# Optimization experiments

Measured on AMD Instinct MI355X. Metric: run time of the kernel, lower is better.

## Reference

```python
import jax, jax.numpy as jnp
import numpy as np

P, L, E, D, NL, FF = 1024, 32, 512, 768, 6, 3072
H_PA, H_TR = 4, 8
VOCAB = 256


def layer_norm(x, w, b, eps=1e-5):
    mu = x.mean(-1, keepdims=True)
    var = ((x - mu) ** 2).mean(-1, keepdims=True)
    return (x - mu) / jnp.sqrt(var + eps) * w + b


def mha(x, wqkv, bqkv, wo, bo, nheads, key_mask=None):
    # x: [B,S,E]; torch nn.MultiheadAttention semantics (scale q by 1/sqrt(d))
    B, S, Emb = x.shape
    d = Emb // nheads
    qkv = x @ wqkv.T + bqkv
    q, k, v = jnp.split(qkv, 3, axis=-1)
    hd = lambda t: t.reshape(B, S, nheads, d).transpose(0, 2, 1, 3)
    q, k, v = hd(q) * (d ** -0.5), hd(k), hd(v)
    scores = jnp.einsum('bhqd,bhkd->bhqk', q, k)
    if key_mask is not None:
        scores = jnp.where(key_mask[:, None, None, :], scores, -1e9)
    a = jax.nn.softmax(scores, axis=-1)
    o = jnp.einsum('bhqk,bhkd->bhqd', a, v).transpose(0, 2, 1, 3).reshape(B, S, Emb)
    return o @ wo.T + bo


def setup_inputs() -> dict:
    key = jax.random.key(0)
    ks = jax.random.split(key, 32)
    n = lambda i, shape, s=0.02: (jax.random.normal(ks[i], shape, dtype=jnp.float32) * s)
    x = lambda i, shape: jax.random.normal(ks[i], shape, dtype=jnp.float32) * (1.0 / np.sqrt(shape[-1]))
    tokens = jax.random.randint(ks[0], (P, L), 0, VOCAB, dtype=jnp.int32)
    lengths = jax.random.randint(ks[1], (P,), 4, L + 1, dtype=jnp.int32)
    byte_emb = n(2, (VOCAB, E)).at[0].set(0.0)  # padding_idx=0
    inp = {
        'tokens': tokens, 'lengths': lengths,
        'byte_emb': byte_emb,
        'local_pos_emb': n(3, (L, E)),
        'patch_pos_emb': n(4, (P, D)),
        'pa_qkv_w': x(5, (3 * E, E)), 'pa_qkv_b': jnp.zeros((3 * E,), jnp.float32),
        'pa_out_w': x(6, (E, E)), 'pa_out_b': jnp.zeros((E,), jnp.float32),
        'proj_w': x(7, (D, E)), 'proj_b': jnp.zeros((D,), jnp.float32),
        'layers_qkv_w': x(8, (NL, 3 * D, D)), 'layers_qkv_b': jnp.zeros((NL, 3 * D), jnp.float32),
        'layers_out_w': x(9, (NL, D, D)), 'layers_out_b': jnp.zeros((NL, D), jnp.float32),
        'layers_ln1_w': jnp.ones((NL, D), jnp.float32), 'layers_ln1_b': jnp.zeros((NL, D), jnp.float32),
        'layers_ln2_w': jnp.ones((NL, D), jnp.float32), 'layers_ln2_b': jnp.zeros((NL, D), jnp.float32),
        'layers_ff1_w': x(10, (NL, FF, D)), 'layers_ff1_b': jnp.zeros((NL, FF), jnp.float32),
        'layers_ff2_w': x(11, (NL, D, FF)), 'layers_ff2_b': jnp.zeros((NL, D), jnp.float32),
        'ln_f_w': jnp.ones((D,), jnp.float32), 'ln_f_b': jnp.zeros((D,), jnp.float32),
    }
    return inp


def reference(tokens, lengths, byte_emb, local_pos_emb, patch_pos_emb,
              pa_qkv_w, pa_qkv_b, pa_out_w, pa_out_b, proj_w, proj_b,
              layers_qkv_w, layers_qkv_b, layers_out_w, layers_out_b,
              layers_ln1_w, layers_ln1_b, layers_ln2_w, layers_ln2_b,
              layers_ff1_w, layers_ff1_b, layers_ff2_w, layers_ff2_b,
              ln_f_w, ln_f_b):
    mask = jnp.arange(L) < lengths[:, None]  # [P,L] valid-byte mask
    # encode_patches: byte embed + local positions, zero padded slots
    emb = byte_emb[tokens] + local_pos_emb[None, :, :]  # [P,L,E]
    emb = emb * mask[..., None].astype(emb.dtype)
    # per-patch MHA over bytes (key padding mask), vectorized across patches
    attn = mha(emb, pa_qkv_w, pa_qkv_b, pa_out_w, pa_out_b, H_PA, key_mask=mask)
    cnt = mask.sum(-1, keepdims=True).astype(emb.dtype)
    patch_repr = (attn * mask[..., None].astype(emb.dtype)).sum(1) / cnt  # [P,E] masked mean
    # project to hidden and add patch-level positions
    h = patch_repr @ proj_w.T + proj_b + patch_pos_emb[:P]
    h = h[None]  # [1,P,D]
    # pre-norm transformer encoder, gelu FFN
    for i in range(NL):
        hn = layer_norm(h, layers_ln1_w[i], layers_ln1_b[i])
        h = h + mha(hn, layers_qkv_w[i], layers_qkv_b[i], layers_out_w[i], layers_out_b[i], H_TR)
        hn = layer_norm(h, layers_ln2_w[i], layers_ln2_b[i])
        ff = jax.nn.gelu(hn @ layers_ff1_w[i].T + layers_ff1_b[i], approximate=False)
        h = h + ff @ layers_ff2_w[i].T + layers_ff2_b[i]
    return layer_norm(h, ln_f_w, ln_f_b)[0]  # [P,D]
```

## Files before the change

### kernel.cpp

```cpp
#include <hip/hip_runtime.h>
#include <hip/hip_bf16.h>
#include <math.h>

typedef __hip_bfloat16 bf16;
typedef unsigned short u16;
typedef __attribute__((ext_vector_type(8))) short short8;
typedef __attribute__((ext_vector_type(4))) float f32x4;
typedef __attribute__((ext_vector_type(4))) unsigned u32x4;

#define PP 1024
#define LL 32
#define EE 512
#define DD 768
#define NLAYER 6
#define FFDIM 3072

__device__ __forceinline__ float bf2f(u16 u) { return __uint_as_float(((unsigned)u) << 16); }
__device__ __forceinline__ u16 f2b(float x) {
  unsigned u = __float_as_uint(x);
  return (u16)((u + 0x7FFFu + ((u >> 16) & 1u)) >> 16);
}

__global__ __launch_bounds__(256) void cvt4(
    const float* s0, const float* s1, const float* s2, const float* s3,
    u16* d0, u16* d1, u16* d2, u16* d3,
    int n0, int n1, int n2, int n3)
{
  int r = blockIdx.y;
  const float* s = r == 0 ? s0 : r == 1 ? s1 : r == 2 ? s2 : s3;
  u16* d        = r == 0 ? d0 : r == 1 ? d1 : r == 2 ? d2 : d3;
  int n4        = r == 0 ? n0 : r == 1 ? n1 : r == 2 ? n2 : n3;
  int i = blockIdx.x * 256 + threadIdx.x;
  if (i < n4) {
    float4 v = ((const float4*)s)[i];
    ushort4 o;
    o.x = f2b(v.x); o.y = f2b(v.y); o.z = f2b(v.z); o.w = f2b(v.w);
    ((ushort4*)d)[i] = o;
  }
}

__global__ __launch_bounds__(256) void embed_table(
    const float* __restrict__ be, const float* __restrict__ lp, bf16* __restrict__ T)
{
  int i = blockIdx.x * 256 + threadIdx.x;
  int r = i >> 6, c = (i & 63) << 3;
  int t = r >> 5, l = r & 31;
  const float* bp = be + ((long)t << 9) + c;
  const float* pp = lp + ((long)l << 9) + c;
  float4 x0 = *(const float4*)bp, x1 = *(const float4*)(bp + 4);
  float4 y0 = *(const float4*)pp, y1 = *(const float4*)(pp + 4);
  short8 o;
  o[0] = (short)f2b(x0.x + y0.x); o[1] = (short)f2b(x0.y + y0.y);
  o[2] = (short)f2b(x0.z + y0.z); o[3] = (short)f2b(x0.w + y0.w);
  o[4] = (short)f2b(x1.x + y1.x); o[5] = (short)f2b(x1.y + y1.y);
  o[6] = (short)f2b(x1.z + y1.z); o[7] = (short)f2b(x1.w + y1.w);
  *(short8*)((u16*)T + ((long)r << 9) + c) = o;
}

__global__ __launch_bounds__(256) void gemm64(
    const bf16* A, long sAb, int lda,
    const bf16* B, long sBb, int ldb,
    float* Cf, bf16* Cb, long sCb, int ldc,
    const float* bias, int biasStride,
    const float* addf,
    int M, int N, int K, int act)
{
  __shared__ u16 As[2][64][72];
  __shared__ u16 Bs[2][64][72];
  const int bz = blockIdx.z;
  const u16* Ap = (const u16*)A + (long)bz * sAb;
  const u16* Bp = (const u16*)B + (long)bz * sBb;
  const long coff = (long)bz * sCb;
  const int m0 = blockIdx.x << 6, n0 = blockIdx.y << 6;
  const int tid = threadIdx.x;
  const int wave = tid >> 6, lane = tid & 63;
  const int sr = tid >> 3;
  const int scc = (tid & 7) << 3;
  const int br0 = n0 + sr, br1 = n0 + sr + 32;
  const short8 zz = {0,0,0,0,0,0,0,0};
  f32x4 acc[4] = {{0.f,0.f,0.f,0.f},{0.f,0.f,0.f,0.f},{0.f,0.f,0.f,0.f},{0.f,0.f,0.f,0.f}};

  {
    int ch = K < 64 ? K : 64;
    bool kv = scc < ch;
    short8 a0 = zz, a1 = zz, b0 = zz, b1 = zz;
    if (kv) {
      a0 = *(const short8*)(Ap + (long)(m0 + sr) * lda + scc);
      a1 = *(const short8*)(Ap + (long)(m0 + sr + 32) * lda + scc);
      if (br0 < N) b0 = *(const short8*)(Bp + (long)br0 * ldb + scc);
      if (br1 < N) b1 = *(const short8*)(Bp + (long)br1 * ldb + scc);
    }
    *(short8*)&As[0][sr][scc] = a0;
    *(short8*)&As[0][sr + 32][scc] = a1;
    *(short8*)&Bs[0][sr][scc] = b0;
    *(short8*)&Bs[0][sr + 32][scc] = b1;
  }
  __syncthreads();

  const int arow = (wave << 4) + (lane & 15);
  const int kq = (lane >> 4) << 3;
  int buf = 0;
  for (int k0 = 0; k0 < K; k0 += 64) {
    int knext = k0 + 64;
    bool more = knext < K;
    short8 a0 = zz, a1 = zz, b0 = zz, b1 = zz;
    if (more) {
      int ch = K - knext; if (ch > 64) ch = 64;
      bool kv = scc < ch;
      if (kv) {
        a0 = *(const short8*)(Ap + (long)(m0 + sr) * lda + knext + scc);
        a1 = *(const short8*)(Ap + (long)(m0 + sr + 32) * lda + knext + scc);
        if (br0 < N) b0 = *(const short8*)(Bp + (long)br0 * ldb + knext + scc);
        if (br1 < N) b1 = *(const short8*)(Bp + (long)br1 * ldb + knext + scc);
      }
    }
    int rem = K - k0; if (rem > 64) rem = 64;
    {
      short8 af = *(const short8*)&As[buf][arow][kq];
#pragma unroll
      for (int nt = 0; nt < 4; nt++) {
        short8 bfr = *(const short8*)&Bs[buf][(nt << 4) + (lane & 15)][kq];
        acc[nt] = __builtin_amdgcn_mfma_f32_16x16x32_bf16(af, bfr, acc[nt], 0, 0, 0);
      }
    }
    if (rem > 32) {
      short8 af = *(const short8*)&As[buf][arow][32 + kq];
#pragma unroll
      for (int nt = 0; nt < 4; nt++) {
        short8 bfr = *(const short8*)&Bs[buf][(nt << 4) + (lane & 15)][32 + kq];
        acc[nt] = __builtin_amdgcn_mfma_f32_16x16x32_bf16(af, bfr, acc[nt], 0, 0, 0);
      }
    }
    if (more) {
      int nb = buf ^ 1;
      *(short8*)&As[nb][sr][scc] = a0;
      *(short8*)&As[nb][sr + 32][scc] = a1;
      *(short8*)&Bs[nb][sr][scc] = b0;
      *(short8*)&Bs[nb][sr + 32][scc] = b1;
      __syncthreads();
      buf = nb;
    }
  }

  int rbase = m0 + (wave << 4) + ((lane >> 4) << 2);
#pragma unroll
  for (int nt = 0; nt < 4; nt++) {
    int c = n0 + (nt << 4) + (lane & 15);
    if (c >= N) continue;
    float bvl = bias ? bias[bz * biasStride + c] : 0.f;
    if (act == 2 && bz != 0) bvl = 0.f;
#pragma unroll
    for (int j = 0; j < 4; j++) {
      int r = rbase + j;
      long idx = coff + (long)r * ldc + c;
      float v = acc[nt][j] + bvl;
      if (addf) v += addf[idx];
      if (act == 1) v = 0.5f * v * (1.f + erff(v * 0.70710678118654752f));
      if (Cf) Cf[idx] = v;
      if (Cb) Cb[idx] = __float2bfloat16(v);
    }
  }
}

__global__ __launch_bounds__(128) void fused_attn(
    const bf16* __restrict__ qkvt,
    const bf16* __restrict__ Vt,
    bf16* __restrict__ attn)
{
  const int h = blockIdx.y;
  const int wid = threadIdx.x >> 6;
  const int lane = threadIdx.x & 63;
  const int q0 = (blockIdx.x << 5) + (wid << 4);
  const int lr = lane & 15;
  const int lq = lane >> 4;
  const float scale = 0.10206207261596577f;

  const u16* qp = (const u16*)qkvt;
  const u16* kp = qp + 768 + h * 96 + (lq << 3);
  const u16* vp = (const u16*)Vt + ((long)(h * 96 + lr) << 10) + (lq << 3);

  short8 qf[3];
#pragma unroll
  for (int c = 0; c < 3; c++)
    qf[c] = *(const short8*)(qp + (long)(q0 + lr) * 2304 + h * 96 + (c << 5) + (lq << 3));

  f32x4 o[6] = {{0.f,0.f,0.f,0.f},{0.f,0.f,0.f,0.f},{0.f,0.f,0.f,0.f},
                {0.f,0.f,0.f,0.f},{0.f,0.f,0.f,0.f},{0.f,0.f,0.f,0.f}};
  float m = -INFINITY, l = 0.f;

  for (int k0 = 0; k0 < 1024; k0 += 32) {
    f32x4 s0 = {0.f,0.f,0.f,0.f}, s1 = {0.f,0.f,0.f,0.f};
#pragma unroll
    for (int c = 0; c < 3; c++) {
      short8 kf0 = *(const short8*)(kp + (long)(k0 + lr) * 2304 + (c << 5));
      short8 kf1 = *(const short8*)(kp + (long)(k0 + 16 + lr) * 2304 + (c << 5));
      s0 = __builtin_amdgcn_mfma_f32_16x16x32_bf16(kf0, qf[c], s0, 0, 0, 0);
      s1 = __builtin_amdgcn_mfma_f32_16x16x32_bf16(kf1, qf[c], s1, 0, 0, 0);
    }
    float e0[4], e1[4];
    float mx = -INFINITY;
#pragma unroll
    for (int r = 0; r < 4; r++) {
      e0[r] = s0[r] * scale;
      e1[r] = s1[r] * scale;
      mx = fmaxf(mx, fmaxf(e0[r], e1[r]));
    }
    mx = fmaxf(mx, __shfl_xor(mx, 16));
    mx = fmaxf(mx, __shfl_xor(mx, 32));
    float mn = fmaxf(m, mx);
    float ts = 0.f;
#pragma unroll
    for (int r = 0; r < 4; r++) {
      e0[r] = __expf(e0[r] - mn);
      e1[r] = __expf(e1[r] - mn);
      ts += e0[r] + e1[r];
    }
    ts += __shfl_xor(ts, 16);
    ts += __shfl_xor(ts, 32);
    if (!__all(mx <= m)) {
      float f = __expf(m - mn);
      float fr[4];
#pragma unroll
      for (int r = 0; r < 4; r++) fr[r] = __shfl(f, (lq << 2) + r);
#pragma unroll
      for (int n = 0; n < 6; n++)
#pragma unroll
        for (int r = 0; r < 4; r++) o[n][r] *= fr[r];
      l *= f;
    }
    l += ts;
    m = mn;

    unsigned a01 = ((unsigned)f2b(e0[1]) << 16) | f2b(e0[0]);
    unsigned a23 = ((unsigned)f2b(e0[3]) << 16) | f2b(e0[2]);
    unsigned b01 = ((unsigned)f2b(e1[1]) << 16) | f2b(e1[0]);
    unsigned b23 = ((unsigned)f2b(e1[3]) << 16) | f2b(e1[2]);
    int sA = lr + ((lq & 1) << 5);
    int sB = sA + 16;
    unsigned qa01 = (unsigned)__shfl((int)a01, sA);
    unsigned qa23 = (unsigned)__shfl((int)a23, sA);
    unsigned qb01 = (unsigned)__shfl((int)b01, sA);
    unsigned qb23 = (unsigned)__shfl((int)b23, sA);
    unsigned ra01 = (unsigned)__shfl((int)a01, sB);
    unsigned ra23 = (unsigned)__shfl((int)a23, sB);
    unsigned rb01 = (unsigned)__shfl((int)b01, sB);
    unsigned rb23 = (unsigned)__shfl((int)b23, sB);
    bool hi = lq >= 2;
    u32x4 wv;
    wv[0] = hi ? qb01 : qa01;
    wv[1] = hi ? qb23 : qa23;
    wv[2] = hi ? rb01 : ra01;
    wv[3] = hi ? rb23 : ra23;
    short8 pa = __builtin_bit_cast(short8, wv);

#pragma unroll
    for (int n = 0; n < 6; n++) {
      short8 vf = *(const short8*)(vp + (long)(n << 4) * 1024 + k0);
      o[n] = __builtin_amdgcn_mfma_f32_16x16x32_bf16(pa, vf, o[n], 0, 0, 0);
    }
  }

  float inv = 1.f / l;
  float ir[4];
#pragma unroll
  for (int r = 0; r < 4; r++) ir[r] = __shfl(inv, (lq << 2) + r);
  u16* op = (u16*)attn + (long)(q0 + (lq << 2)) * 768 + h * 96 + lr;
#pragma unroll
  for (int r = 0; r < 4; r++)
#pragma unroll
    for (int n = 0; n < 6; n++)
      op[(long)r * 768 + (n << 4)] = f2b(o[n][r] * ir[r]);
}

__global__ __launch_bounds__(256) void patch_attn(
    const bf16* __restrict__ qkt,
    const int* __restrict__ tokens, const int* __restrict__ lengths,
    const float* __restrict__ byte_emb, const float* __restrict__ local_pos,
    bf16* __restrict__ Z)
{
  __shared__ float wsum[4][32];
  __shared__ int tok_s[32];
  __shared__ int cnt_s;
  int p = blockIdx.x;
  int tid = threadIdx.x;
  if (tid < 32) tok_s[tid] = tokens[p * 32 + tid];
  if (tid == 0) cnt_s = lengths[p];
  __syncthreads();
  int cnt = cnt_s;
  int h = tid >> 6, lane = tid & 63;
  const int rsel = lane & 15;
  const int ksel = (lane >> 4) << 3;
  const u16* qkb = (const u16*)qkt + h * 128;
  const long r0 = ((long)((tok_s[rsel] << 5) | rsel)) << 10;
  const long r1 = ((long)((tok_s[16 + rsel] << 5) | (16 + rsel))) << 10;

  f32x4 acc[2][2] = {{{0.f,0.f,0.f,0.f},{0.f,0.f,0.f,0.f}},
                     {{0.f,0.f,0.f,0.f},{0.f,0.f,0.f,0.f}}};
#pragma unroll
  for (int kc = 0; kc < 4; kc++) {
    int ko = kc * 32 + ksel;
    short8 a0 = *(const short8*)(qkb + r0 + ko);
    short8 a1 = *(const short8*)(qkb + r1 + ko);
    short8 b0 = *(const short8*)(qkb + r0 + 512 + ko);
    short8 b1 = *(const short8*)(qkb + r1 + 512 + ko);
    acc[0][0] = __builtin_amdgcn_mfma_f32_16x16x32_bf16(a0, b0, acc[0][0], 0, 0, 0);
    acc[0][1] = __builtin_amdgcn_mfma_f32_16x16x32_bf16(a0, b1, acc[0][1], 0, 0, 0);
    acc[1][0] = __builtin_amdgcn_mfma_f32_16x16x32_bf16(a1, b0, acc[1][0], 0, 0, 0);
    acc[1][1] = __builtin_amdgcn_mfma_f32_16x16x32_bf16(a1, b1, acc[1][1], 0, 0, 0);
  }

  const float scale = 0.088388347648318447f;
  int j0 = lane & 15, j1 = 16 + j0;
  bool v0 = j0 < cnt, v1 = j1 < cnt;
  int rowq = (lane >> 4) << 2;
  float cs0 = 0.f, cs1 = 0.f;
#pragma unroll
  for (int ti = 0; ti < 2; ti++) {
    float s0[4], s1[4], mx[4], sm[4], e0[4], e1[4];
#pragma unroll
    for (int r = 0; r < 4; r++) {
      s0[r] = acc[ti][0][r] * scale;
      s1[r] = acc[ti][1][r] * scale;
      float a = v0 ? s0[r] : -1e30f;
      float b = v1 ? s1[r] : -1e30f;
      mx[r] = fmaxf(a, b);
    }
#pragma unroll
    for (int d = 1; d < 16; d <<= 1)
#pragma unroll
      for (int r = 0; r < 4; r++) mx[r] = fmaxf(mx[r], __shfl_xor(mx[r], d));
#pragma unroll
    for (int r = 0; r < 4; r++) {
      e0[r] = v0 ? __expf(s0[r] - mx[r]) : 0.f;
      e1[r] = v1 ? __expf(s1[r] - mx[r]) : 0.f;
      sm[r] = e0[r] + e1[r];
    }
#pragma unroll
    for (int d = 1; d < 16; d <<= 1)
#pragma unroll
      for (int r = 0; r < 4; r++) sm[r] += __shfl_xor(sm[r], d);
#pragma unroll
    for (int r = 0; r < 4; r++) {
      int row = ti * 16 + rowq + r;
      if (row < cnt) {
        float inv = 1.f / sm[r];
        cs0 += e0[r] * inv;
        cs1 += e1[r] * inv;
      }
    }
  }
  cs0 += __shfl_xor(cs0, 16); cs0 += __shfl_xor(cs0, 32);
  cs1 += __shfl_xor(cs1, 16); cs1 += __shfl_xor(cs1, 32);
  if (lane < 16) {
    float invc = 1.f / (float)cnt;
    wsum[h][lane] = cs0 * invc;
    wsum[h][16 + lane] = cs1 * invc;
  }
  __syncthreads();

  for (int e = tid; e < 512; e += 256) {
    float za0 = 0.f, za1 = 0.f, za2 = 0.f, za3 = 0.f;
    for (int j = 0; j < cnt; j++) {
      float ev = byte_emb[((long)tok_s[j] << 9) + e] + local_pos[((long)j << 9) + e];
      za0 += wsum[0][j] * ev;
      za1 += wsum[1][j] * ev;
      za2 += wsum[2][j] * ev;
      za3 += wsum[3][j] * ev;
    }
    long zb = (long)p * 2048;
    Z[zb + e]        = __float2bfloat16(za0);
    Z[zb + 512 + e]  = __float2bfloat16(za1);
    Z[zb + 1024 + e] = __float2bfloat16(za2);
    Z[zb + 1536 + e] = __float2bfloat16(za3);
  }
}

__global__ __launch_bounds__(256) void ln_kernel(
    const float* __restrict__ x,
    const float* __restrict__ a0, const float* __restrict__ a1,
    const float* __restrict__ a2, const float* __restrict__ a3,
    float* __restrict__ hout,
    const float* __restrict__ w, const float* __restrict__ b,
    bf16* outb, float* outf)
{
  __shared__ float red[8];
  __shared__ float mv[2];
  int row = blockIdx.x;
  long base = (long)row * DD;
  int tid = threadIdx.x, lane = tid & 63, wave = tid >> 6;
  float vv[3];
  float s = 0.f, s2 = 0.f;
#pragma unroll
  for (int j = 0; j < 3; j++) {
    long c = base + tid + j * 256;
    float v = x[c];
    if (a0) v += a0[c];
    if (a1) v += a1[c];
    if (a2) v += a2[c];
    if (a3) v += a3[c];
    if (hout) hout[c] = v;
    vv[j] = v; s += v; s2 += v * v;
  }
  for (int o = 32; o; o >>= 1) { s += __shfl_down(s, o); s2 += __shfl_down(s2, o); }
  if (lane == 0) { red[wave] = s; red[4 + wave] = s2; }
  __syncthreads();
  if (tid == 0) {
    float ts = red[0] + red[1] + red[2] + red[3];
    float ts2 = red[4] + red[5] + red[6] + red[7];
    float mu = ts / DD;
    float var = ts2 / DD - mu * mu;
    mv[0] = mu; mv[1] = rsqrtf(var + 1e-5f);
  }
  __syncthreads();
  float mu = mv[0], rstd = mv[1];
#pragma unroll
  for (int j = 0; j < 3; j++) {
    int c = tid + j * 256;
    float v = (vv[j] - mu) * rstd * w[c] + b[c];
    if (outb) outb[base + c] = __float2bfloat16(v);
    if (outf) outf[base + c] = v;
  }
}

__global__ __launch_bounds__(256) void transpose_v(
    const bf16* __restrict__ qkv, bf16* __restrict__ Vt)
{
  __shared__ u16 tile[32][33];
  int k0 = blockIdx.x << 5;
  int d0 = blockIdx.y << 5;
  int tx = threadIdx.x & 31, ty = threadIdx.x >> 5;
  const u16* q = (const u16*)qkv;
  for (int i = ty; i < 32; i += 8)
    tile[i][tx] = q[(long)(k0 + i) * 2304 + 1536 + d0 + tx];
  __syncthreads();
  u16* vt = (u16*)Vt;
  for (int i = ty; i < 32; i += 8)
    vt[(long)(d0 + i) * 1024 + k0 + tx] = tile[tx][i];
}

extern "C" void kernel_launch(void* const* d_in, const int* in_sizes, int n_in,
                              void* d_out, int out_size, void* d_ws, size_t ws_size,
                              hipStream_t stream)
{
  const int*   tokens    = (const int*)d_in[0];
  const int*   lengths   = (const int*)d_in[1];
  const float* byte_emb  = (const float*)d_in[2];
  const float* local_pos = (const float*)d_in[3];
  const float* patch_pos = (const float*)d_in[4];
  const float* pa_qkv_w  = (const float*)d_in[5];
  const float* pa_qkv_b  = (const float*)d_in[6];
  const float* pa_out_w  = (const float*)d_in[7];
  const float* pa_out_b  = (const float*)d_in[8];
  const float* proj_w    = (const float*)d_in[9];
  const float* proj_b    = (const float*)d_in[10];
  const float* Wqkv      = (const float*)d_in[11];
  const float* Bqkv      = (const float*)d_in[12];
  const float* Wout      = (const float*)d_in[13];
  const float* Bout      = (const float*)d_in[14];
  const float* ln1w      = (const float*)d_in[15];
  const float* ln1b      = (const float*)d_in[16];
  const float* ln2w      = (const float*)d_in[17];
  const float* ln2b      = (const float*)d_in[18];
  const float* W1        = (const float*)d_in[19];
  const float* B1        = (const float*)d_in[20];
  const float* W2        = (const float*)d_in[21];
  const float* B2        = (const float*)d_in[22];
  const float* lnfw      = (const float*)d_in[23];
  const float* lnfb      = (const float*)d_in[24];

  char* ws = (char*)d_ws;
  const size_t MB = 1ull << 20;
  bf16* qkT    = (bf16*)(ws);
  bf16* qkvt   = (bf16*)(ws + 16 * MB);
  bf16* Vt     = (bf16*)(ws + 21 * MB);
  bf16* attn   = (bf16*)(ws + 23 * MB);
  bf16* ffb    = (bf16*)(ws + 25 * MB);
  float* h     = (float*)(ws + 31 * MB);
  bf16* hn     = (bf16*)(ws + 34 * MB);
  u16*  Lw     = (u16*)(ws + 36 * MB);
  bf16* embT   = (bf16*)(ws + 50 * MB);
  float* hp    = (float*)(ws + 58 * MB);
  bf16* Z      = (bf16*)(ws + 64 * MB);
  bf16* o_mean = (bf16*)(ws + 68 * MB);
  bf16* t1     = (bf16*)(ws + 69 * MB);
  u16*  P1w    = (u16*)(ws + 70 * MB);

  const long PSTRIDE = (long)PP * DD;

  const long oLQKV = 0;
  const long oLOUT = 1769472;
  const long oLW1  = 2359296;
  const long oLW2  = 4718592;
  const long oPAQ  = 0;
  const long oPAO  = 786432;
  const long oPRJ  = 1048576;

  cvt4<<<dim3(768, 3), 256, 0, stream>>>(
      pa_qkv_w, pa_out_w, proj_w, nullptr,
      P1w + oPAQ, P1w + oPAO, P1w + oPRJ, nullptr,
      786432 / 4, 262144 / 4, 393216 / 4, 0);
  embed_table<<<2048, 256, 0, stream>>>(byte_emb, local_pos, embT);
  gemm64<<<dim3(128, 16, 1), 256, 0, stream>>>(
      embT, 0, EE, (bf16*)(P1w + oPAQ), 0, EE, nullptr, qkT, 0, 1024,
      pa_qkv_b, 0, nullptr, 8192, 1024, EE, 0);
  patch_attn<<<PP, 256, 0, stream>>>(
      qkT, tokens, lengths, byte_emb, local_pos, Z);
  gemm64<<<dim3(16, 2, 4), 256, 0, stream>>>(
      Z, 512, 2048, (bf16*)(P1w + oPAQ + 1024L * EE), 128L * EE, EE,
      nullptr, o_mean, 128, EE, pa_qkv_b + 1024, 128, nullptr, PP, 128, EE, 0);
  gemm64<<<dim3(16, 8, 1), 256, 0, stream>>>(
      o_mean, 0, EE, (bf16*)(P1w + oPAO), 0, EE, nullptr, t1, 0, EE,
      pa_out_b, 0, nullptr, PP, EE, EE, 0);
  gemm64<<<dim3(16, 12, 1), 256, 0, stream>>>(
      t1, 0, EE, (bf16*)(P1w + oPRJ), 0, EE, h, nullptr, 0, DD,
      proj_b, 0, patch_pos, PP, DD, EE, 0);

  for (int i = 0; i < NLAYER; i++) {
    cvt4<<<dim3(2304, 4), 256, 0, stream>>>(
        Wqkv + (long)i * 2304 * DD, Wout + (long)i * DD * DD,
        W1 + (long)i * FFDIM * DD, W2 + (long)i * DD * FFDIM,
        Lw + oLQKV, Lw + oLOUT, Lw + oLW1, Lw + oLW2,
        1769472 / 4, 589824 / 4, 2359296 / 4, 2359296 / 4);
    if (i == 0)
      ln_kernel<<<PP, 256, 0, stream>>>(h, nullptr, nullptr, nullptr, nullptr,
                                        nullptr, ln1w + i * DD, ln1b + i * DD, hn, nullptr);
    else
      ln_kernel<<<PP, 256, 0, stream>>>(h, hp, hp + PSTRIDE, hp + 2 * PSTRIDE, hp + 3 * PSTRIDE,
                                        h, ln1w + i * DD, ln1b + i * DD, hn, nullptr);
    gemm64<<<dim3(16, 36, 1), 256, 0, stream>>>(
        hn, 0, DD, (bf16*)(Lw + oLQKV), 0, DD, nullptr, qkvt, 0, 2304,
        Bqkv + i * 2304, 0, nullptr, PP, 2304, DD, 0);
    transpose_v<<<dim3(32, 24), 256, 0, stream>>>(qkvt, Vt);
    fused_attn<<<dim3(32, 8), 128, 0, stream>>>(qkvt, Vt, attn);
    gemm64<<<dim3(16, 12, 2), 256, 0, stream>>>(
        attn, 384, DD, (bf16*)(Lw + oLOUT), 384, DD, hp, nullptr, PSTRIDE, DD,
        Bout + i * DD, 0, nullptr, PP, DD, 384, 2);
    ln_kernel<<<PP, 256, 0, stream>>>(h, hp, hp + PSTRIDE, nullptr, nullptr,
                                      h, ln2w + i * DD, ln2b + i * DD, hn, nullptr);
    gemm64<<<dim3(16, 48, 1), 256, 0, stream>>>(
        hn, 0, DD, (bf16*)(Lw + oLW1), 0, DD, nullptr, ffb, 0, FFDIM,
        B1 + i * FFDIM, 0, nullptr, PP, FFDIM, DD, 1);
    gemm64<<<dim3(16, 12, 4), 256, 0, stream>>>(
        ffb, 768, FFDIM, (bf16*)(Lw + oLW2), 768, FFDIM, hp, nullptr, PSTRIDE, DD,
        B2 + i * DD, 0, nullptr, PP, DD, 768, 2);
  }
  ln_kernel<<<PP, 256, 0, stream>>>(h, hp, hp + PSTRIDE, hp + 2 * PSTRIDE, hp + 3 * PSTRIDE,
                                    nullptr, lnfw, lnfb, nullptr, (float*)d_out);
}
```

Baseline: 1.010 ms.

## Split attention over key chunks with a separate log-sum-exp combine kernel

The fused attention kernel now splits the 1024 keys into four chunks along a new grid dimension. Each chunk writes unnormalized fp32 partial outputs plus its running max and sum into scratch, reusing the hp buffer and the freed P1w region. A new combine kernel merges the four partials with log-sum-exp weights and writes the bf16 attention output. The goal is to fill more compute units than the original 256 small blocks did, at the cost of an extra launch and extra fp32 traffic to global memory.

```diff
diff --git a/kernel.cpp b/kernel.cpp
--- a/kernel.cpp
+++ b/kernel.cpp
@@ -165,14 +165,18 @@
 __global__ __launch_bounds__(128) void fused_attn(
     const bf16* __restrict__ qkvt,
     const bf16* __restrict__ Vt,
-    bf16* __restrict__ attn)
+    float* __restrict__ Op,
+    float* __restrict__ marr,
+    float* __restrict__ larr)
 {
   const int h = blockIdx.y;
+  const int ks = blockIdx.z;
   const int wid = threadIdx.x >> 6;
   const int lane = threadIdx.x & 63;
   const int q0 = (blockIdx.x << 5) + (wid << 4);
   const int lr = lane & 15;
   const int lq = lane >> 4;
+  const int kbase = ks << 8;
   const float scale = 0.10206207261596577f;
 
   const u16* qp = (const u16*)qkvt;
@@ -188,7 +192,7 @@
                 {0.f,0.f,0.f,0.f},{0.f,0.f,0.f,0.f},{0.f,0.f,0.f,0.f}};
   float m = -INFINITY, l = 0.f;
 
-  for (int k0 = 0; k0 < 1024; k0 += 32) {
+  for (int k0 = kbase; k0 < kbase + 256; k0 += 32) {
     f32x4 s0 = {0.f,0.f,0.f,0.f}, s1 = {0.f,0.f,0.f,0.f};
 #pragma unroll
     for (int c = 0; c < 3; c++) {
@@ -260,16 +264,39 @@
     }
   }
 
-  float inv = 1.f / l;
-  float ir[4];
-#pragma unroll
-  for (int r = 0; r < 4; r++) ir[r] = __shfl(inv, (lq << 2) + r);
-  u16* op = (u16*)attn + (long)(q0 + (lq << 2)) * 768 + h * 96 + lr;
+  float* Opf = Op + (long)(ks * 8 + h) * 98304;
 #pragma unroll
   for (int r = 0; r < 4; r++)
 #pragma unroll
     for (int n = 0; n < 6; n++)
-      op[(long)r * 768 + (n << 4)] = f2b(o[n][r] * ir[r]);
+      Opf[(long)(q0 + (lq << 2) + r) * 96 + (n << 4) + lr] = o[n][r];
+  if (lq == 0) {
+    int idx = (ks * 8 + h) * 1024 + q0 + lr;
+    marr[idx] = m;
+    larr[idx] = l;
+  }
+}
+
+__global__ __launch_bounds__(128) void attn_combine(
+    const float* __restrict__ Op, const float* __restrict__ marr,
+    const float* __restrict__ larr, bf16* __restrict__ attn)
+{
+  int q = blockIdx.x, h = blockIdx.y;
+  int t = threadIdx.x;
+  int base = h * 1024 + q;
+  float m0 = marr[base], m1 = marr[8192 + base];
+  float m2 = marr[16384 + base], m3 = marr[24576 + base];
+  float M = fmaxf(fmaxf(m0, m1), fmaxf(m2, m3));
+  float w0 = __expf(m0 - M), w1 = __expf(m1 - M);
+  float w2 = __expf(m2 - M), w3 = __expf(m3 - M);
+  float L = larr[base] * w0 + larr[8192 + base] * w1
+          + larr[16384 + base] * w2 + larr[24576 + base] * w3;
+  if (t < 96) {
+    long o = (long)base * 96 + t;
+    float v = Op[o] * w0 + Op[786432 + o] * w1
+            + Op[1572864 + o] * w2 + Op[2359296 + o] * w3;
+    ((u16*)attn)[(long)q * 768 + h * 96 + t] = f2b(v / L);
+  }
 }
 
 __global__ __launch_bounds__(256) void patch_attn(
@@ -484,6 +511,8 @@
   bf16* o_mean = (bf16*)(ws + 68 * MB);
   bf16* t1     = (bf16*)(ws + 69 * MB);
   u16*  P1w    = (u16*)(ws + 70 * MB);
+  float* marr  = (float*)(ws + 70 * MB);
+  float* larr  = (float*)(ws + 70 * MB + 131072);
 
   const long PSTRIDE = (long)PP * DD;
 
@@ -531,7 +560,8 @@
         hn, 0, DD, (bf16*)(Lw + oLQKV), 0, DD, nullptr, qkvt, 0, 2304,
         Bqkv + i * 2304, 0, nullptr, PP, 2304, DD, 0);
     transpose_v<<<dim3(32, 24), 256, 0, stream>>>(qkvt, Vt);
-    fused_attn<<<dim3(32, 8), 128, 0, stream>>>(qkvt, Vt, attn);
+    fused_attn<<<dim3(32, 8, 4), 128, 0, stream>>>(qkvt, Vt, hp, marr, larr);
+    attn_combine<<<dim3(1024, 8), 128, 0, stream>>>(hp, marr, larr, attn);
     gemm64<<<dim3(16, 12, 2), 256, 0, stream>>>(
         attn, 384, DD, (bf16*)(Lw + oLOUT), 384, DD, hp, nullptr, PSTRIDE, DD,
         Bout + i * DD, 0, nullptr, PP, DD, 384, 2);
```

Measured after the change: 975.2 us. 1.04x faster.
